# Kernel tuning notes

Measured on AMD Instinct MI355X. Metric: run time of the kernel, lower is better.

Reference implementation:

```python
import jax, jax.numpy as jnp
import numpy as np

B, T, H, K, C, U, IN = 128, 800, 512, 10, 80, 64, 3


def setup_inputs() -> dict:
    key = jax.random.key(0)
    ks = jax.random.split(key, 6)
    s = 0.08  # small init so exp() window params stay stable
    return {
        "strokes": jax.random.normal(ks[0], (B, T, IN), jnp.float32),
        "sentences": jax.random.randint(ks[1], (B, U), 0, C),
        "sentences_mask": jnp.ones((B, U), jnp.float32),
        "W_ih": jax.random.normal(ks[2], (4 * H, IN + C), jnp.float32) * s,
        "W_hh": jax.random.normal(ks[3], (4 * H, H), jnp.float32) * s,
        "b_ih": jnp.zeros((4 * H,), jnp.float32),
        "b_hh": jnp.zeros((4 * H,), jnp.float32),
        "W_win": jax.random.normal(ks[4], (3 * K, H), jnp.float32) * s,
        "b_win": jnp.zeros((3 * K,), jnp.float32),
    }


def reference(strokes, sentences, sentences_mask, W_ih, W_hh, b_ih, b_hh, W_win, b_win):
    # Pre-mask the one-hot character encoding: [B, U, C]
    onehot = jax.nn.one_hot(sentences, C, dtype=jnp.float32) * sentences_mask[:, :, None]
    u = jnp.arange(U, dtype=jnp.float32)  # character position grid
    bias = b_ih + b_hh

    def step(carry, x_t):
        h, c, kappa_prev, window = carry
        inp = jnp.concatenate([x_t, window], axis=-1)           # [B, IN+C]
        gates = inp @ W_ih.T + h @ W_hh.T + bias                 # [B, 4H]
        i, f, g, o = jnp.split(gates, 4, axis=-1)                # torch LSTMCell order i,f,g,o
        i, f, o = jax.nn.sigmoid(i), jax.nn.sigmoid(f), jax.nn.sigmoid(o)
        c = f * c + i * jnp.tanh(g)
        h = o * jnp.tanh(c)
        # Gaussian window parameters (eq. 48-51 in Graves 2013)
        p = h @ W_win.T + b_win                                  # [B, 3K]
        a_hat, b_hat, k_hat = jnp.split(p, 3, axis=-1)
        alpha = jnp.exp(a_hat)
        beta = jnp.exp(b_hat)
        kappa = kappa_prev + jnp.exp(k_hat)
        # phi[b,u] = sum_k alpha * exp(-beta * (kappa - u)^2)
        d = kappa[:, :, None] - u[None, None, :]                 # [B, K, U]
        phi = jnp.sum(alpha[:, :, None] * jnp.exp(-beta[:, :, None] * d * d), axis=1)  # [B, U]
        window = jnp.einsum('bu,buc->bc', phi, onehot)           # [B, C]
        return (h, c, kappa, window), (h, window, phi)

    init = (
        jnp.zeros((B, H), jnp.float32),
        jnp.zeros((B, H), jnp.float32),
        jnp.zeros((B, K), jnp.float32),
        jnp.zeros((B, C), jnp.float32),
    )
    xs = jnp.swapaxes(strokes, 0, 1)                             # [T, B, IN]
    _, (h_seq, w_seq, phi_seq) = jax.lax.scan(step, init, xs)
    return (
        jnp.swapaxes(h_seq, 0, 1),    # [B, T, H]
        jnp.swapaxes(w_seq, 0, 1),    # [B, T, C]
        jnp.swapaxes(phi_seq, 0, 1),  # [B, T, U]
    )
```

## Files before the change

### kernel.cpp

```cpp
#include <hip/hip_runtime.h>
#include <hip/hip_bf16.h>
#include <math.h>

#define B_   128
#define T_   800
#define H_   512
#define K_   10
#define C_   80
#define U_   64
#define IN_  3

#define NG   4
#define BPG  64
#define BT   32
#define NT   256
#define KROW 608
#define HB   512

#define WS_PACC_F  (2*B_*HB)
#define WS_BAR_F   (WS_PACC_F + NG*BT*30*2)
#define WS_TOTAL_F (WS_BAR_F + NG*8*32)

#define OFF_H    0ull
#define OFF_W    ((size_t)B_ * T_ * H_)
#define OFF_PHI  (OFF_W + (size_t)B_ * T_ * C_)

typedef __attribute__((ext_vector_type(8))) short short8;
typedef __attribute__((ext_vector_type(4))) float f32x4;

#define SWZB(row)    (((row) ^ ((row) >> 2)) & 3)
#define SWIDX(row,k) ((row)*KROW + ((((k) >> 3) ^ SWZB(row)) << 3) + ((k) & 7))
#define LDFRAG(arr,row,u) (*(const short8*)&(arr)[(row)*KROW + (((u) ^ SWZB(row)) << 3)])

__device__ __forceinline__ void stb_u32(unsigned* p, unsigned v) {
  asm volatile("global_store_dword %0, %1, off sc0 sc1" :: "v"(p), "v"(v) : "memory");
}
__device__ __forceinline__ void fence_vm() {
  asm volatile("s_waitcnt vmcnt(0)" ::: "memory");
}
__device__ __forceinline__ void flag_add(unsigned* p) {
  __hip_atomic_fetch_add(p, 1u, __ATOMIC_RELAXED, __HIP_MEMORY_SCOPE_AGENT);
}
__device__ __forceinline__ unsigned flag_ld(unsigned* p) {
  return __hip_atomic_load(p, __ATOMIC_RELAXED, __HIP_MEMORY_SCOPE_AGENT);
}
__device__ __forceinline__ void acq_fence(unsigned* p) {
  (void)__hip_atomic_load(p, __ATOMIC_ACQUIRE, __HIP_MEMORY_SCOPE_AGENT);
}
__device__ __forceinline__ float sigmoidf_(float v) { return 1.0f / (1.0f + expf(-v)); }
__device__ __forceinline__ unsigned pack_hl(float v) {
  unsigned hb = __float_as_uint(v) >> 16;
  float rs = v - __uint_as_float(hb << 16);
  unsigned lb = __float_as_uint(rs) >> 16;
  return (hb << 16) | lb;
}
__device__ __forceinline__ float comb_hl(short h, short l) {
  return __uint_as_float((unsigned)(unsigned short)h << 16) +
         __uint_as_float((unsigned)(unsigned short)l << 16);
}

__global__ void __launch_bounds__(256, 2)
init_ws_kernel(float* __restrict__ ws) {
  size_t i = (size_t)blockIdx.x * 256 + threadIdx.x;
  const size_t n = (size_t)WS_TOTAL_F;
  const size_t stride = (size_t)gridDim.x * 256;
  for (; i < n; i += stride) ws[i] = 0.0f;
}

__global__ void __launch_bounds__(NT, 1)
graves_kernel(const float* __restrict__ x,
              const int*   __restrict__ sent,
              const float* __restrict__ smask,
              const float* __restrict__ W_ih,
              const float* __restrict__ W_hh,
              const float* __restrict__ b_ih,
              const float* __restrict__ b_hh,
              const float* __restrict__ W_win,
              const float* __restrict__ b_win,
              float* __restrict__ out,
              float* __restrict__ ws)
{
  const int tid = threadIdx.x;
  const int bid = blockIdx.x;
  const int g   = bid >> 6;
  const int ub  = bid & (BPG - 1);
  const int b0  = g * BT;
  const int u0  = ub * 8;

  unsigned*  gbuf   = (unsigned*)ws;
  long long* pacc_g = (long long*)(ws + WS_PACC_F) + (size_t)g * (BT * 30);
  unsigned*  fb     = (unsigned*)(ws + WS_BAR_F) + (size_t)g * 256;
  unsigned*  c1l    = fb;

  __shared__ __align__(16) short whi[32 * KROW];
  __shared__ __align__(16) short wlo[32 * KROW];
  __shared__ __align__(16) short shi[32 * KROW];
  __shared__ __align__(16) short slo[32 * KROW];
  __shared__ float pbufS[32][32];
  __shared__ float hT[8 * 32];
  __shared__ float wwin[8 * 30];
  __shared__ float xwb[32 * 4];
  float* pbf = &pbufS[0][0];

  for (int idx = tid; idx < 32 * KROW; idx += NT) {
    const int r = idx / KROW, k = idx - r * KROW;
    const int uu = r >> 2, gate = r & 3, gr = gate * H_ + u0 + uu;
    float wv = 0.0f;
    if (k < H_)           wv = W_hh[(size_t)gr * H_ + k];
    else if (k < H_ + C_) wv = W_ih[(size_t)gr * (IN_ + C_) + IN_ + (k - H_)];
    const unsigned hb = __float_as_uint(wv) >> 16;
    const float rs = wv - __uint_as_float(hb << 16);
    const unsigned lb = __float_as_uint(rs) >> 16;
    const int li = SWIDX(r, k);
    whi[li] = (short)hb;
    wlo[li] = (short)lb;
  }
  for (int idx = tid; idx < 32 * 16; idx += NT) {
    const int b2 = idx >> 4, k = (H_ + C_) + (idx & 15);
    shi[SWIDX(b2, k)] = 0; slo[SWIDX(b2, k)] = 0;
  }
  if (tid < 32) {
    const int uu = tid >> 2, gate = tid & 3, gr = gate * H_ + u0 + uu;
    xwb[tid * 4 + 0] = W_ih[(size_t)gr * (IN_ + C_) + 0];
    xwb[tid * 4 + 1] = W_ih[(size_t)gr * (IN_ + C_) + 1];
    xwb[tid * 4 + 2] = W_ih[(size_t)gr * (IN_ + C_) + 2];
    xwb[tid * 4 + 3] = b_ih[gr] + b_hh[gr];
  }
  for (int idx = tid; idx < 240; idx += NT) {
    const int uu = idx / 30, j = idx - uu * 30;
    wwin[idx] = W_win[(size_t)j * H_ + u0 + uu];
  }

  const int lane = tid & 63;
  const int wid  = tid >> 6;
  const int ni   = wid & 1;
  const int kh   = wid >> 1;
  const int r16  = lane & 15;
  const int g4   = lane >> 4;
  const int bb   = ni * 16 + r16;

  const int pb = tid >> 3, ug = tid & 7;
  float msk[8]; int snt[8];
  #pragma unroll
  for (int i = 0; i < 8; ++i) {
    msk[i] = smask[(size_t)(b0 + pb) * U_ + ug * 8 + i];
    snt[i] = sent [(size_t)(b0 + pb) * U_ + ug * 8 + i];
  }
  const bool isWriter = (ub < BT);
  const int  wb_b = b0 + ub;
  __syncthreads();

  float cr0 = 0.0f, cr1 = 0.0f;
  long long prevp[4] = {0, 0, 0, 0};
  float kprevf[4] = {0.f, 0.f, 0.f, 0.f};

#define GSTEP(ks) { \
    const int uu_ = (ks) * 4 + g4; \
    const short8 bh = LDFRAG(shi, bb, uu_); \
    const short8 bl = LDFRAG(slo, bb, uu_); \
    const short8 ah0 = LDFRAG(whi, r16, uu_); \
    const short8 al0 = LDFRAG(wlo, r16, uu_); \
    const short8 ah1 = LDFRAG(whi, 16 + r16, uu_); \
    const short8 al1 = LDFRAG(wlo, 16 + r16, uu_); \
    a0 = __builtin_amdgcn_mfma_f32_16x16x32_bf16(ah0, bh, a0, 0, 0, 0); \
    a0 = __builtin_amdgcn_mfma_f32_16x16x32_bf16(ah0, bl, a0, 0, 0, 0); \
    a0 = __builtin_amdgcn_mfma_f32_16x16x32_bf16(al0, bh, a0, 0, 0, 0); \
    a1 = __builtin_amdgcn_mfma_f32_16x16x32_bf16(ah1, bh, a1, 0, 0, 0); \
    a1 = __builtin_amdgcn_mfma_f32_16x16x32_bf16(ah1, bl, a1, 0, 0, 0); \
    a1 = __builtin_amdgcn_mfma_f32_16x16x32_bf16(al1, bh, a1, 0, 0, 0); \
  }

  for (int t = 0; t <= T_; ++t) {
    if (t == T_ && !isWriter) break;

    const unsigned* pIn  = gbuf + (size_t)((t & 1) ^ 1) * (B_ * HB);
    unsigned*       pOut = gbuf + (size_t)(t & 1) * (B_ * HB);

    if (t > 0 && tid < 4) {
      unsigned* line = c1l + tid * 32;
      const unsigned tgt = 16u * (unsigned)t;
      while (flag_ld(line) < tgt) __builtin_amdgcn_s_sleep(1);
      acq_fence(line);
    }
    __syncthreads();

    float xv0 = 0.f, xv1 = 0.f, xv2 = 0.f;
    {
      const int sb = tid & 31, seg = tid >> 5;
      const unsigned* grow = pIn + (size_t)(b0 + sb) * HB + seg * 64;
      uint4 v[16];
      #pragma unroll
      for (int i = 0; i < 16; ++i) v[i] = *(const uint4*)(grow + i * 4);
      #pragma unroll
      for (int i = 0; i < 16; ++i) {
        const int k = seg * 64 + i * 4;
        const int idx = SWIDX(sb, k);
        const unsigned h01 = (v[i].x >> 16) | ((v[i].y >> 16) << 16);
        const unsigned h23 = (v[i].z >> 16) | ((v[i].w >> 16) << 16);
        const unsigned l01 = (v[i].x & 0xffffu) | ((v[i].y & 0xffffu) << 16);
        const unsigned l23 = (v[i].z & 0xffffu) | ((v[i].w & 0xffffu) << 16);
        *(uint2*)&shi[idx] = make_uint2(h01, h23);
        *(uint2*)&slo[idx] = make_uint2(l01, l23);
      }
      #pragma unroll
      for (int i = 0; i < 10; ++i) {
        const int c = seg * 10 + i;
        const int idx = SWIDX(sb, H_ + c);
        shi[idx] = 0; slo[idx] = 0;
      }
      if (kh == 0 && t < T_) {
        const float* xp = x + ((size_t)(b0 + bb) * T_ + t) * IN_;
        xv0 = xp[0]; xv1 = xp[1]; xv2 = xp[2];
      }
    }
    __syncthreads();

    if (t >= 1) {
      #pragma unroll
      for (int r = 0; r < 4; ++r) {
        const int item = tid + 256 * r;
        if (item < 960) {
          const int b = item / 30, j = item - b * 30;
          const long long v = pacc_g[b * 30 + j];
          const int hi = (int)(v >> 32);
          const unsigned lo = (unsigned)(v & 0xffffffffLL);
          const float pv = (float)hi + (float)lo * 0x1p-32f + b_win[j];
          float ev = __expf(pv);
          if (j >= 20) { ev += kprevf[r]; kprevf[r] = ev; }
          pbufS[b][j] = ev;
        }
      }
      __syncthreads();

      float al[10], be[10], ka[10];
      #pragma unroll
      for (int k2 = 0; k2 < 10; ++k2) {
        al[k2] = pbufS[pb][k2];
        be[k2] = pbufS[pb][10 + k2];
        ka[k2] = pbufS[pb][20 + k2];
      }
      float ph[8];
      #pragma unroll
      for (int i = 0; i < 8; ++i) {
        const float fu = (float)(ug * 8 + i);
        float s = 0.0f;
        #pragma unroll
        for (int k2 = 0; k2 < 10; ++k2) {
          const float d = ka[k2] - fu;
          s = fmaf(al[k2], __expf(-be[k2] * d * d), s);
        }
        ph[i] = s;
      }
      if (isWriter && pb == ub) {
        #pragma unroll
        for (int i = 0; i < 8; ++i)
          out[OFF_PHI + ((size_t)wb_b * T_ + (t - 1)) * U_ + ug * 8 + i] = ph[i];
      }
      #pragma unroll
      for (int i = 0; i < 8; ++i) ph[i] *= msk[i];

      #pragma unroll
      for (int r = 0; r < 8; ++r) {
        if (ug == r) {
          #pragma unroll
          for (int i = 0; i < 8; ++i) {
            const int idx = SWIDX(pb, H_ + snt[i]);
            float cur = comb_hl(shi[idx], slo[idx]) + ph[i];
            const unsigned pk = pack_hl(cur);
            shi[idx] = (short)(pk >> 16);
            slo[idx] = (short)(pk & 0xffffu);
          }
        }
        asm volatile("" ::: "memory");
      }
      __syncthreads();
      if (isWriter && tid < C_) {
        const int idx = SWIDX(ub, H_ + tid);
        out[OFF_W + ((size_t)wb_b * T_ + (t - 1)) * C_ + tid] = comb_hl(shi[idx], slo[idx]);
      }
    }
    if (t == T_) break;

    f32x4 a0 = {0.f, 0.f, 0.f, 0.f}, a1 = {0.f, 0.f, 0.f, 0.f};
    if (kh == 0) {
      #pragma unroll
      for (int ks = 0; ks < 8; ++ks) GSTEP(ks);
      GSTEP(16);
    } else {
      #pragma unroll
      for (int ks = 8; ks < 16; ++ks) GSTEP(ks);
      GSTEP(17); GSTEP(18);
    }

    __syncthreads();
    if (kh == 1) {
      #pragma unroll
      for (int e = 0; e < 4; ++e) {
        pbf[(ni * 2 + 0) * 256 + (g4 * 4 + e) * 16 + r16] = a0[e];
        pbf[(ni * 2 + 1) * 256 + (g4 * 4 + e) * 16 + r16] = a1[e];
      }
    }
    __syncthreads();
    if (kh == 0) {
      #pragma unroll
      for (int mi = 0; mi < 2; ++mi) {
        float ge[4];
        #pragma unroll
        for (int e = 0; e < 4; ++e) {
          const int r = mi * 16 + g4 * 4 + e;
          const float av = ((mi == 0) ? a0[e] : a1[e]) + pbf[(ni * 2 + mi) * 256 + (g4 * 4 + e) * 16 + r16];
          ge[e] = av + xwb[r*4+0]*xv0 + xwb[r*4+1]*xv1 + xwb[r*4+2]*xv2 + xwb[r*4+3];
        }
        const float iv = sigmoidf_(ge[0]);
        const float fv = sigmoidf_(ge[1]);
        const float gv = tanhf(ge[2]);
        const float ov = sigmoidf_(ge[3]);
        const float cprev = (mi == 0) ? cr0 : cr1;
        const float cv = fmaf(fv, cprev, iv * gv);
        if (mi == 0) cr0 = cv; else cr1 = cv;
        const float hv = ov * tanhf(cv);
        const int uu = mi * 4 + g4;
        hT[uu * 32 + bb] = hv;
        stb_u32(&pOut[(size_t)(b0 + bb) * HB + (u0 + uu)], pack_hl(hv));
        out[OFF_H + ((size_t)(b0 + bb) * T_ + t) * H_ + (u0 + uu)] = hv;
      }
    }
    __syncthreads();

    #pragma unroll
    for (int r = 0; r < 4; ++r) {
      const int item = tid + 256 * r;
      if (item < 960) {
        const int b = item / 30, j = item - b * 30;
        float s = 0.0f;
        #pragma unroll
        for (int uu = 0; uu < 8; ++uu) s = fmaf(wwin[uu * 30 + j], hT[uu * 32 + b], s);
        const long long nv = llrintf(s * 4294967296.0f);
        const unsigned long long d = (unsigned long long)(nv - prevp[r]);
        prevp[r] = nv;
        __hip_atomic_fetch_add((unsigned long long*)(pacc_g + b * 30 + j), d,
                               __ATOMIC_RELAXED, __HIP_MEMORY_SCOPE_AGENT);
      }
    }
    fence_vm();
    __syncthreads();
    if (tid == 0) flag_add(c1l + (ub & 3) * 32);
  }
#undef GSTEP
}

extern "C" void kernel_launch(void* const* d_in, const int* in_sizes, int n_in,
                              void* d_out, int out_size, void* d_ws, size_t ws_size,
                              hipStream_t stream) {
  const float* x     = (const float*)d_in[0];
  const int*   sent  = (const int*)  d_in[1];
  const float* smask = (const float*)d_in[2];
  const float* W_ih  = (const float*)d_in[3];
  const float* W_hh  = (const float*)d_in[4];
  const float* b_ih  = (const float*)d_in[5];
  const float* b_hh  = (const float*)d_in[6];
  const float* W_win = (const float*)d_in[7];
  const float* b_win = (const float*)d_in[8];
  float* ws  = (float*)d_ws;
  float* out = (float*)d_out;

  hipLaunchKernelGGL(init_ws_kernel, dim3(512), dim3(256), 0, stream, ws);
  hipLaunchKernelGGL(graves_kernel, dim3(NG * BPG), dim3(NT), 0, stream,
                     x, sent, smask, W_ih, W_hh, b_ih, b_hh, W_win, b_win, out, ws);
}
```

Before: 11.77 ms.

## Register-resident weights, sharded double-buffered window accumulators, wider flag lines

```diff
diff --git a/kernel.cpp b/kernel.cpp
--- a/kernel.cpp
+++ b/kernel.cpp
@@ -16,9 +16,10 @@
 #define NT   256
 #define KROW 608
 #define HB   512
+#define SHARDS 8
 
 #define WS_PACC_F  (2*B_*HB)
-#define WS_BAR_F   (WS_PACC_F + NG*BT*30*2)
+#define WS_BAR_F   (WS_PACC_F + 2*NG*SHARDS*960*2)
 #define WS_TOTAL_F (WS_BAR_F + NG*8*32)
 
 #define OFF_H    0ull
@@ -87,13 +88,11 @@
   const int b0  = g * BT;
   const int u0  = ub * 8;
 
-  unsigned*  gbuf   = (unsigned*)ws;
-  long long* pacc_g = (long long*)(ws + WS_PACC_F) + (size_t)g * (BT * 30);
-  unsigned*  fb     = (unsigned*)(ws + WS_BAR_F) + (size_t)g * 256;
-  unsigned*  c1l    = fb;
-
-  __shared__ __align__(16) short whi[32 * KROW];
-  __shared__ __align__(16) short wlo[32 * KROW];
+  unsigned*  gbuf      = (unsigned*)ws;
+  long long* pacc_base = (long long*)(ws + WS_PACC_F);
+  unsigned*  fb        = (unsigned*)(ws + WS_BAR_F) + (size_t)g * 256;
+  unsigned*  c1l       = fb;
+
   __shared__ __align__(16) short shi[32 * KROW];
   __shared__ __align__(16) short slo[32 * KROW];
   __shared__ float pbufS[32][32];
@@ -102,35 +101,6 @@
   __shared__ float xwb[32 * 4];
   float* pbf = &pbufS[0][0];
 
-  for (int idx = tid; idx < 32 * KROW; idx += NT) {
-    const int r = idx / KROW, k = idx - r * KROW;
-    const int uu = r >> 2, gate = r & 3, gr = gate * H_ + u0 + uu;
-    float wv = 0.0f;
-    if (k < H_)           wv = W_hh[(size_t)gr * H_ + k];
-    else if (k < H_ + C_) wv = W_ih[(size_t)gr * (IN_ + C_) + IN_ + (k - H_)];
-    const unsigned hb = __float_as_uint(wv) >> 16;
-    const float rs = wv - __uint_as_float(hb << 16);
-    const unsigned lb = __float_as_uint(rs) >> 16;
-    const int li = SWIDX(r, k);
-    whi[li] = (short)hb;
-    wlo[li] = (short)lb;
-  }
-  for (int idx = tid; idx < 32 * 16; idx += NT) {
-    const int b2 = idx >> 4, k = (H_ + C_) + (idx & 15);
-    shi[SWIDX(b2, k)] = 0; slo[SWIDX(b2, k)] = 0;
-  }
-  if (tid < 32) {
-    const int uu = tid >> 2, gate = tid & 3, gr = gate * H_ + u0 + uu;
-    xwb[tid * 4 + 0] = W_ih[(size_t)gr * (IN_ + C_) + 0];
-    xwb[tid * 4 + 1] = W_ih[(size_t)gr * (IN_ + C_) + 1];
-    xwb[tid * 4 + 2] = W_ih[(size_t)gr * (IN_ + C_) + 2];
-    xwb[tid * 4 + 3] = b_ih[gr] + b_hh[gr];
-  }
-  for (int idx = tid; idx < 240; idx += NT) {
-    const int uu = idx / 30, j = idx - uu * 30;
-    wwin[idx] = W_win[(size_t)j * H_ + u0 + uu];
-  }
-
   const int lane = tid & 63;
   const int wid  = tid >> 6;
   const int ni   = wid & 1;
@@ -139,6 +109,57 @@
   const int g4   = lane >> 4;
   const int bb   = ni * 16 + r16;
 
+  for (int idx = tid; idx < 32 * 16; idx += NT) {
+    const int b2 = idx >> 4, k = (H_ + C_) + (idx & 15);
+    shi[SWIDX(b2, k)] = 0; slo[SWIDX(b2, k)] = 0;
+  }
+  if (tid < 32) {
+    const int uu = tid >> 2, gate = tid & 3, gr = gate * H_ + u0 + uu;
+    xwb[tid * 4 + 0] = W_ih[(size_t)gr * (IN_ + C_) + 0];
+    xwb[tid * 4 + 1] = W_ih[(size_t)gr * (IN_ + C_) + 1];
+    xwb[tid * 4 + 2] = W_ih[(size_t)gr * (IN_ + C_) + 2];
+    xwb[tid * 4 + 3] = b_ih[gr] + b_hh[gr];
+  }
+  for (int idx = tid; idx < 240; idx += NT) {
+    const int uu = idx / 30, j = idx - uu * 30;
+    wwin[idx] = W_win[(size_t)j * H_ + u0 + uu];
+  }
+
+  short8 wah[10], wal[10], wbh[10], wbl[10];
+  {
+    const int uuA = r16 >> 2, gateA = r16 & 3;
+    const int grA = gateA * H_ + u0 + uuA;
+    const int grB = gateA * H_ + u0 + 4 + uuA;
+    #pragma unroll
+    for (int slot = 0; slot < 10; ++slot) {
+      int ks = 0; bool act;
+      if (kh == 0) { act = (slot < 9); ks = (slot < 8) ? slot : 16; }
+      else         { act = true;       ks = (slot < 8) ? (8 + slot) : ((slot == 8) ? 17 : 18); }
+      short8 h0 = {0,0,0,0,0,0,0,0}, l0 = h0, h1 = h0, l1 = h0;
+      if (act) {
+        #pragma unroll
+        for (int e = 0; e < 8; ++e) {
+          const int k = ks * 32 + g4 * 8 + e;
+          float wA = 0.f, wB = 0.f;
+          if (k < H_) {
+            wA = W_hh[(size_t)grA * H_ + k];
+            wB = W_hh[(size_t)grB * H_ + k];
+          } else if (k < H_ + C_) {
+            wA = W_ih[(size_t)grA * (IN_ + C_) + IN_ + (k - H_)];
+            wB = W_ih[(size_t)grB * (IN_ + C_) + IN_ + (k - H_)];
+          }
+          const unsigned ha = __float_as_uint(wA) >> 16;
+          const float ra = wA - __uint_as_float(ha << 16);
+          h0[e] = (short)ha; l0[e] = (short)(__float_as_uint(ra) >> 16);
+          const unsigned hbb = __float_as_uint(wB) >> 16;
+          const float rb = wB - __uint_as_float(hbb << 16);
+          h1[e] = (short)hbb; l1[e] = (short)(__float_as_uint(rb) >> 16);
+        }
+      }
+      wah[slot] = h0; wal[slot] = l0; wbh[slot] = h1; wbl[slot] = l1;
+    }
+  }
+
   const int pb = tid >> 3, ug = tid & 7;
   float msk[8]; int snt[8];
   #pragma unroll
@@ -151,24 +172,34 @@
   __syncthreads();
 
   float cr0 = 0.0f, cr1 = 0.0f;
-  long long prevp[4] = {0, 0, 0, 0};
   float kprevf[4] = {0.f, 0.f, 0.f, 0.f};
-
-#define GSTEP(ks) { \
-    const int uu_ = (ks) * 4 + g4; \
+  long long pA0 = 0, pA1 = 0, pA2 = 0, pA3 = 0;
+  long long pB0 = 0, pB1 = 0, pB2 = 0, pB3 = 0;
+
+#define GSTEP(slot, ksv) { \
+    const int uu_ = (ksv) * 4 + g4; \
     const short8 bh = LDFRAG(shi, bb, uu_); \
     const short8 bl = LDFRAG(slo, bb, uu_); \
-    const short8 ah0 = LDFRAG(whi, r16, uu_); \
-    const short8 al0 = LDFRAG(wlo, r16, uu_); \
-    const short8 ah1 = LDFRAG(whi, 16 + r16, uu_); \
-    const short8 al1 = LDFRAG(wlo, 16 + r16, uu_); \
-    a0 = __builtin_amdgcn_mfma_f32_16x16x32_bf16(ah0, bh, a0, 0, 0, 0); \
-    a0 = __builtin_amdgcn_mfma_f32_16x16x32_bf16(ah0, bl, a0, 0, 0, 0); \
-    a0 = __builtin_amdgcn_mfma_f32_16x16x32_bf16(al0, bh, a0, 0, 0, 0); \
-    a1 = __builtin_amdgcn_mfma_f32_16x16x32_bf16(ah1, bh, a1, 0, 0, 0); \
-    a1 = __builtin_amdgcn_mfma_f32_16x16x32_bf16(ah1, bl, a1, 0, 0, 0); \
-    a1 = __builtin_amdgcn_mfma_f32_16x16x32_bf16(al1, bh, a1, 0, 0, 0); \
-  }
+    a0 = __builtin_amdgcn_mfma_f32_16x16x32_bf16(wah[slot], bh, a0, 0, 0, 0); \
+    a0 = __builtin_amdgcn_mfma_f32_16x16x32_bf16(wah[slot], bl, a0, 0, 0, 0); \
+    a0 = __builtin_amdgcn_mfma_f32_16x16x32_bf16(wal[slot], bh, a0, 0, 0, 0); \
+    a1 = __builtin_amdgcn_mfma_f32_16x16x32_bf16(wbh[slot], bh, a1, 0, 0, 0); \
+    a1 = __builtin_amdgcn_mfma_f32_16x16x32_bf16(wbh[slot], bl, a1, 0, 0, 0); \
+    a1 = __builtin_amdgcn_mfma_f32_16x16x32_bf16(wbl[slot], bh, a1, 0, 0, 0); \
+  }
+
+#define PUB1(r, PREV) { \
+    const int item = tid + 256 * (r); \
+    if (item < 960) { \
+      const int b2 = item / 30, j = item - b2 * 30; \
+      float s = 0.f; \
+      _Pragma("unroll") \
+      for (int uu = 0; uu < 8; ++uu) s = fmaf(wwin[uu * 30 + j], hT[uu * 32 + b2], s); \
+      const long long nv = llrintf(s * 4294967296.0f); \
+      const unsigned long long d = (unsigned long long)(nv - (PREV)); \
+      (PREV) = nv; \
+      __hip_atomic_fetch_add(paccW + item, d, __ATOMIC_RELAXED, __HIP_MEMORY_SCOPE_AGENT); \
+    } }
 
   for (int t = 0; t <= T_; ++t) {
     if (t == T_ && !isWriter) break;
@@ -176,9 +207,9 @@
     const unsigned* pIn  = gbuf + (size_t)((t & 1) ^ 1) * (B_ * HB);
     unsigned*       pOut = gbuf + (size_t)(t & 1) * (B_ * HB);
 
-    if (t > 0 && tid < 4) {
+    if (t > 0 && tid < 8) {
       unsigned* line = c1l + tid * 32;
-      const unsigned tgt = 16u * (unsigned)t;
+      const unsigned tgt = 8u * (unsigned)t;
       while (flag_ld(line) < tgt) __builtin_amdgcn_s_sleep(1);
       acq_fence(line);
     }
@@ -216,18 +247,21 @@
     __syncthreads();
 
     if (t >= 1) {
+      const long long* paccR = pacc_base + ((size_t)(((t - 1) & 1) * NG + g) * SHARDS) * 960;
       #pragma unroll
       for (int r = 0; r < 4; ++r) {
         const int item = tid + 256 * r;
         if (item < 960) {
-          const int b = item / 30, j = item - b * 30;
-          const long long v = pacc_g[b * 30 + j];
+          long long v = 0;
+          #pragma unroll
+          for (int sh = 0; sh < SHARDS; ++sh) v += paccR[(size_t)sh * 960 + item];
           const int hi = (int)(v >> 32);
           const unsigned lo = (unsigned)(v & 0xffffffffLL);
+          const int b2 = item / 30, j = item - b2 * 30;
           const float pv = (float)hi + (float)lo * 0x1p-32f + b_win[j];
           float ev = __expf(pv);
           if (j >= 20) { ev += kprevf[r]; kprevf[r] = ev; }
-          pbufS[b][j] = ev;
+          pbufS[b2][j] = ev;
         }
       }
       __syncthreads();
@@ -283,13 +317,13 @@
 
     f32x4 a0 = {0.f, 0.f, 0.f, 0.f}, a1 = {0.f, 0.f, 0.f, 0.f};
     if (kh == 0) {
-      #pragma unroll
-      for (int ks = 0; ks < 8; ++ks) GSTEP(ks);
-      GSTEP(16);
+      GSTEP(0, 0) GSTEP(1, 1) GSTEP(2, 2) GSTEP(3, 3)
+      GSTEP(4, 4) GSTEP(5, 5) GSTEP(6, 6) GSTEP(7, 7)
+      GSTEP(8, 16)
     } else {
-      #pragma unroll
-      for (int ks = 8; ks < 16; ++ks) GSTEP(ks);
-      GSTEP(17); GSTEP(18);
+      GSTEP(0, 8)  GSTEP(1, 9)  GSTEP(2, 10) GSTEP(3, 11)
+      GSTEP(4, 12) GSTEP(5, 13) GSTEP(6, 14) GSTEP(7, 15)
+      GSTEP(8, 17) GSTEP(9, 18)
     }
 
     __syncthreads();
@@ -322,31 +356,30 @@
         const int uu = mi * 4 + g4;
         hT[uu * 32 + bb] = hv;
         stb_u32(&pOut[(size_t)(b0 + bb) * HB + (u0 + uu)], pack_hl(hv));
-        out[OFF_H + ((size_t)(b0 + bb) * T_ + t) * H_ + (u0 + uu)] = hv;
-      }
-    }
-    __syncthreads();
-
-    #pragma unroll
-    for (int r = 0; r < 4; ++r) {
-      const int item = tid + 256 * r;
-      if (item < 960) {
-        const int b = item / 30, j = item - b * 30;
-        float s = 0.0f;
-        #pragma unroll
-        for (int uu = 0; uu < 8; ++uu) s = fmaf(wwin[uu * 30 + j], hT[uu * 32 + b], s);
-        const long long nv = llrintf(s * 4294967296.0f);
-        const unsigned long long d = (unsigned long long)(nv - prevp[r]);
-        prevp[r] = nv;
-        __hip_atomic_fetch_add((unsigned long long*)(pacc_g + b * 30 + j), d,
-                               __ATOMIC_RELAXED, __HIP_MEMORY_SCOPE_AGENT);
-      }
+      }
+    }
+    __syncthreads();
+
+    {
+      unsigned long long* paccW = (unsigned long long*)
+          (pacc_base + ((size_t)((t & 1) * NG + g) * SHARDS + (ub & 7)) * 960);
+      if (t & 1) { PUB1(0, pB0) PUB1(1, pB1) PUB1(2, pB2) PUB1(3, pB3) }
+      else       { PUB1(0, pA0) PUB1(1, pA1) PUB1(2, pA2) PUB1(3, pA3) }
     }
     fence_vm();
     __syncthreads();
-    if (tid == 0) flag_add(c1l + (ub & 3) * 32);
+    if (tid == 0) flag_add(c1l + (ub & 7) * 32);
+
+    if (kh == 0) {
+      #pragma unroll
+      for (int mi = 0; mi < 2; ++mi) {
+        const int uu = mi * 4 + g4;
+        out[OFF_H + ((size_t)(b0 + bb) * T_ + t) * H_ + (u0 + uu)] = hT[uu * 32 + bb];
+      }
+    }
   }
 #undef GSTEP
+#undef PUB1
 }
 
 extern "C" void kernel_launch(void* const* d_in, const int* in_sizes, int n_in,
```

Measured after the change: 16.36 ms. +39.1%, slower.

## Repartition recurrence into fewer larger blocks with register-resident weights

Applied to the files above, without the earlier changes.

```diff
diff --git a/kernel.cpp b/kernel.cpp
--- a/kernel.cpp
+++ b/kernel.cpp
@@ -11,15 +11,15 @@
 #define IN_  3
 
 #define NG   4
-#define BPG  64
+#define BPG  16
 #define BT   32
-#define NT   256
+#define NT   512
 #define KROW 608
 #define HB   512
 
-#define WS_PACC_F  (2*B_*HB)
-#define WS_BAR_F   (WS_PACC_F + NG*BT*30*2)
-#define WS_TOTAL_F (WS_BAR_F + NG*8*32)
+#define WS_PPS_F   (2*B_*HB)
+#define WS_BAR_F   (WS_PPS_F + 2*NG*BPG*960)
+#define WS_TOTAL_F (WS_BAR_F + NG*4*32)
 
 #define OFF_H    0ull
 #define OFF_W    ((size_t)B_ * T_ * H_)
@@ -35,14 +35,21 @@
 __device__ __forceinline__ void stb_u32(unsigned* p, unsigned v) {
   asm volatile("global_store_dword %0, %1, off sc0 sc1" :: "v"(p), "v"(v) : "memory");
 }
+__device__ __forceinline__ void stb_f32(float* p, float v) {
+  asm volatile("global_store_dword %0, %1, off sc0 sc1" :: "v"(p), "v"(v) : "memory");
+}
 __device__ __forceinline__ void fence_vm() {
   asm volatile("s_waitcnt vmcnt(0)" ::: "memory");
 }
 __device__ __forceinline__ void flag_add(unsigned* p) {
   __hip_atomic_fetch_add(p, 1u, __ATOMIC_RELAXED, __HIP_MEMORY_SCOPE_AGENT);
 }
-__device__ __forceinline__ unsigned flag_ld(unsigned* p) {
-  return __hip_atomic_load(p, __ATOMIC_RELAXED, __HIP_MEMORY_SCOPE_AGENT);
+__device__ __forceinline__ unsigned flag_sum4(unsigned* base) {
+  unsigned s0 = __hip_atomic_load(base +  0, __ATOMIC_RELAXED, __HIP_MEMORY_SCOPE_AGENT);
+  unsigned s1 = __hip_atomic_load(base + 32, __ATOMIC_RELAXED, __HIP_MEMORY_SCOPE_AGENT);
+  unsigned s2 = __hip_atomic_load(base + 64, __ATOMIC_RELAXED, __HIP_MEMORY_SCOPE_AGENT);
+  unsigned s3 = __hip_atomic_load(base + 96, __ATOMIC_RELAXED, __HIP_MEMORY_SCOPE_AGENT);
+  return (s0 + s1) + (s2 + s3);
 }
 __device__ __forceinline__ void acq_fence(unsigned* p) {
   (void)__hip_atomic_load(p, __ATOMIC_ACQUIRE, __HIP_MEMORY_SCOPE_AGENT);
@@ -67,7 +74,7 @@
   for (; i < n; i += stride) ws[i] = 0.0f;
 }
 
-__global__ void __launch_bounds__(NT, 1)
+__global__ void __launch_bounds__(NT, 2)
 graves_kernel(const float* __restrict__ x,
               const int*   __restrict__ sent,
               const float* __restrict__ smask,
@@ -82,153 +89,157 @@
 {
   const int tid = threadIdx.x;
   const int bid = blockIdx.x;
-  const int g   = bid >> 6;
-  const int ub  = bid & (BPG - 1);
-  const int b0  = g * BT;
-  const int u0  = ub * 8;
-
-  unsigned*  gbuf   = (unsigned*)ws;
-  long long* pacc_g = (long long*)(ws + WS_PACC_F) + (size_t)g * (BT * 30);
-  unsigned*  fb     = (unsigned*)(ws + WS_BAR_F) + (size_t)g * 256;
-  unsigned*  c1l    = fb;
-
-  __shared__ __align__(16) short whi[32 * KROW];
-  __shared__ __align__(16) short wlo[32 * KROW];
+  const int xcd  = bid & 7, slot = bid >> 3;
+  const int g    = xcd >> 1;
+  const int ub   = ((xcd & 1) << 3) | slot;
+  const int b0   = g * BT;
+  const int u0   = ub * 32;
+
+  unsigned* gbuf = (unsigned*)ws;
+  float*    pps  = ws + WS_PPS_F;
+  unsigned* c1l  = (unsigned*)(ws + WS_BAR_F) + (size_t)g * 128;
+
   __shared__ __align__(16) short shi[32 * KROW];
   __shared__ __align__(16) short slo[32 * KROW];
   __shared__ float pbufS[32][32];
-  __shared__ float hT[8 * 32];
-  __shared__ float wwin[8 * 30];
-  __shared__ float xwb[32 * 4];
-  float* pbf = &pbufS[0][0];
-
-  for (int idx = tid; idx < 32 * KROW; idx += NT) {
-    const int r = idx / KROW, k = idx - r * KROW;
-    const int uu = r >> 2, gate = r & 3, gr = gate * H_ + u0 + uu;
-    float wv = 0.0f;
-    if (k < H_)           wv = W_hh[(size_t)gr * H_ + k];
-    else if (k < H_ + C_) wv = W_ih[(size_t)gr * (IN_ + C_) + IN_ + (k - H_)];
-    const unsigned hb = __float_as_uint(wv) >> 16;
-    const float rs = wv - __uint_as_float(hb << 16);
-    const unsigned lb = __float_as_uint(rs) >> 16;
-    const int li = SWIDX(r, k);
-    whi[li] = (short)hb;
-    wlo[li] = (short)lb;
-  }
+  __shared__ float hT[32 * 32];
+  __shared__ float wwin[32 * 30];
+  __shared__ float xwb[128][4];
+
+  const int lane = tid & 63;
+  const int wid  = tid >> 6;
+  const int r16  = lane & 15;
+  const int g4   = lane >> 4;
+
   for (int idx = tid; idx < 32 * 16; idx += NT) {
     const int b2 = idx >> 4, k = (H_ + C_) + (idx & 15);
     shi[SWIDX(b2, k)] = 0; slo[SWIDX(b2, k)] = 0;
   }
-  if (tid < 32) {
+  if (tid < 128) {
     const int uu = tid >> 2, gate = tid & 3, gr = gate * H_ + u0 + uu;
-    xwb[tid * 4 + 0] = W_ih[(size_t)gr * (IN_ + C_) + 0];
-    xwb[tid * 4 + 1] = W_ih[(size_t)gr * (IN_ + C_) + 1];
-    xwb[tid * 4 + 2] = W_ih[(size_t)gr * (IN_ + C_) + 2];
-    xwb[tid * 4 + 3] = b_ih[gr] + b_hh[gr];
-  }
-  for (int idx = tid; idx < 240; idx += NT) {
+    xwb[tid][0] = W_ih[(size_t)gr * (IN_ + C_) + 0];
+    xwb[tid][1] = W_ih[(size_t)gr * (IN_ + C_) + 1];
+    xwb[tid][2] = W_ih[(size_t)gr * (IN_ + C_) + 2];
+    xwb[tid][3] = b_ih[gr] + b_hh[gr];
+  }
+  for (int idx = tid; idx < 32 * 30; idx += NT) {
     const int uu = idx / 30, j = idx - uu * 30;
     wwin[idx] = W_win[(size_t)j * H_ + u0 + uu];
   }
 
-  const int lane = tid & 63;
-  const int wid  = tid >> 6;
-  const int ni   = wid & 1;
-  const int kh   = wid >> 1;
-  const int r16  = lane & 15;
-  const int g4   = lane >> 4;
-  const int bb   = ni * 16 + r16;
-
-  const int pb = tid >> 3, ug = tid & 7;
-  float msk[8]; int snt[8];
+  short8 wh[19], wl[19];
+  {
+    const int lrow = wid * 16 + r16;
+    const int uuA = lrow >> 2, gateA = lrow & 3;
+    const int gr = gateA * H_ + u0 + uuA;
+    #pragma unroll
+    for (int ks = 0; ks < 19; ++ks) {
+      short8 h8 = {0,0,0,0,0,0,0,0}, l8 = h8;
+      #pragma unroll
+      for (int e = 0; e < 8; ++e) {
+        const int k = ks * 32 + g4 * 8 + e;
+        float wv = 0.0f;
+        if (k < H_)           wv = W_hh[(size_t)gr * H_ + k];
+        else if (k < H_ + C_) wv = W_ih[(size_t)gr * (IN_ + C_) + IN_ + (k - H_)];
+        const unsigned hb = __float_as_uint(wv) >> 16;
+        const float rs = wv - __uint_as_float(hb << 16);
+        h8[e] = (short)hb; l8[e] = (short)(__float_as_uint(rs) >> 16);
+      }
+      wh[ks] = h8; wl[ks] = l8;
+    }
+  }
+
+  const int pb = tid >> 4, q = tid & 15;
+  float msk[4]; int snt[4];
   #pragma unroll
-  for (int i = 0; i < 8; ++i) {
-    msk[i] = smask[(size_t)(b0 + pb) * U_ + ug * 8 + i];
-    snt[i] = sent [(size_t)(b0 + pb) * U_ + ug * 8 + i];
-  }
-  const bool isWriter = (ub < BT);
-  const int  wb_b = b0 + ub;
+  for (int i = 0; i < 4; ++i) {
+    msk[i] = smask[(size_t)(b0 + pb) * U_ + q * 4 + i];
+    snt[i] = sent [(size_t)(b0 + pb) * U_ + q * 4 + i];
+  }
   __syncthreads();
 
   float cr0 = 0.0f, cr1 = 0.0f;
-  long long prevp[4] = {0, 0, 0, 0};
-  float kprevf[4] = {0.f, 0.f, 0.f, 0.f};
+  float kp0 = 0.0f, kp1 = 0.0f;
 
 #define GSTEP(ks) { \
     const int uu_ = (ks) * 4 + g4; \
-    const short8 bh = LDFRAG(shi, bb, uu_); \
-    const short8 bl = LDFRAG(slo, bb, uu_); \
-    const short8 ah0 = LDFRAG(whi, r16, uu_); \
-    const short8 al0 = LDFRAG(wlo, r16, uu_); \
-    const short8 ah1 = LDFRAG(whi, 16 + r16, uu_); \
-    const short8 al1 = LDFRAG(wlo, 16 + r16, uu_); \
-    a0 = __builtin_amdgcn_mfma_f32_16x16x32_bf16(ah0, bh, a0, 0, 0, 0); \
-    a0 = __builtin_amdgcn_mfma_f32_16x16x32_bf16(ah0, bl, a0, 0, 0, 0); \
-    a0 = __builtin_amdgcn_mfma_f32_16x16x32_bf16(al0, bh, a0, 0, 0, 0); \
-    a1 = __builtin_amdgcn_mfma_f32_16x16x32_bf16(ah1, bh, a1, 0, 0, 0); \
-    a1 = __builtin_amdgcn_mfma_f32_16x16x32_bf16(ah1, bl, a1, 0, 0, 0); \
-    a1 = __builtin_amdgcn_mfma_f32_16x16x32_bf16(al1, bh, a1, 0, 0, 0); \
+    const short8 bh0 = LDFRAG(shi, r16, uu_); \
+    const short8 bl0 = LDFRAG(slo, r16, uu_); \
+    const short8 bh1 = LDFRAG(shi, 16 + r16, uu_); \
+    const short8 bl1 = LDFRAG(slo, 16 + r16, uu_); \
+    a0 = __builtin_amdgcn_mfma_f32_16x16x32_bf16(wh[ks], bh0, a0, 0, 0, 0); \
+    a0 = __builtin_amdgcn_mfma_f32_16x16x32_bf16(wh[ks], bl0, a0, 0, 0, 0); \
+    a0 = __builtin_amdgcn_mfma_f32_16x16x32_bf16(wl[ks], bh0, a0, 0, 0, 0); \
+    a1 = __builtin_amdgcn_mfma_f32_16x16x32_bf16(wh[ks], bh1, a1, 0, 0, 0); \
+    a1 = __builtin_amdgcn_mfma_f32_16x16x32_bf16(wh[ks], bl1, a1, 0, 0, 0); \
+    a1 = __builtin_amdgcn_mfma_f32_16x16x32_bf16(wl[ks], bh1, a1, 0, 0, 0); \
   }
 
   for (int t = 0; t <= T_; ++t) {
-    if (t == T_ && !isWriter) break;
-
     const unsigned* pIn  = gbuf + (size_t)((t & 1) ^ 1) * (B_ * HB);
     unsigned*       pOut = gbuf + (size_t)(t & 1) * (B_ * HB);
 
-    if (t > 0 && tid < 4) {
-      unsigned* line = c1l + tid * 32;
+    if (t > 0 && tid == 0) {
       const unsigned tgt = 16u * (unsigned)t;
-      while (flag_ld(line) < tgt) __builtin_amdgcn_s_sleep(1);
-      acq_fence(line);
+      while (flag_sum4(c1l) < tgt) __builtin_amdgcn_s_sleep(1);
+      acq_fence(c1l);
     }
     __syncthreads();
 
-    float xv0 = 0.f, xv1 = 0.f, xv2 = 0.f;
+    float xv00=0.f,xv01=0.f,xv02=0.f, xv10=0.f,xv11=0.f,xv12=0.f;
     {
       const int sb = tid & 31, seg = tid >> 5;
-      const unsigned* grow = pIn + (size_t)(b0 + sb) * HB + seg * 64;
-      uint4 v[16];
-      #pragma unroll
-      for (int i = 0; i < 16; ++i) v[i] = *(const uint4*)(grow + i * 4);
-      #pragma unroll
-      for (int i = 0; i < 16; ++i) {
-        const int k = seg * 64 + i * 4;
-        const int idx = SWIDX(sb, k);
-        const unsigned h01 = (v[i].x >> 16) | ((v[i].y >> 16) << 16);
-        const unsigned h23 = (v[i].z >> 16) | ((v[i].w >> 16) << 16);
-        const unsigned l01 = (v[i].x & 0xffffu) | ((v[i].y & 0xffffu) << 16);
-        const unsigned l23 = (v[i].z & 0xffffu) | ((v[i].w & 0xffffu) << 16);
-        *(uint2*)&shi[idx] = make_uint2(h01, h23);
-        *(uint2*)&slo[idx] = make_uint2(l01, l23);
-      }
-      #pragma unroll
-      for (int i = 0; i < 10; ++i) {
-        const int c = seg * 10 + i;
+      if (t < T_) {
+        const uint4* grow = (const uint4*)(pIn + (size_t)(b0 + sb) * HB + seg * 32);
+        uint4 v[8];
+        #pragma unroll
+        for (int i = 0; i < 8; ++i) v[i] = grow[i];
+        #pragma unroll
+        for (int i = 0; i < 8; ++i) {
+          const int k = seg * 32 + i * 4;
+          const int idx = SWIDX(sb, k);
+          const unsigned h01 = (v[i].x >> 16) | ((v[i].y >> 16) << 16);
+          const unsigned h23 = (v[i].z >> 16) | ((v[i].w >> 16) << 16);
+          const unsigned l01 = (v[i].x & 0xffffu) | ((v[i].y & 0xffffu) << 16);
+          const unsigned l23 = (v[i].z & 0xffffu) | ((v[i].w & 0xffffu) << 16);
+          *(uint2*)&shi[idx] = make_uint2(h01, h23);
+          *(uint2*)&slo[idx] = make_uint2(l01, l23);
+        }
+        const float* xp0 = x + ((size_t)(b0 + r16) * T_ + t) * IN_;
+        const float* xp1 = x + ((size_t)(b0 + 16 + r16) * T_ + t) * IN_;
+        xv00 = xp0[0]; xv01 = xp0[1]; xv02 = xp0[2];
+        xv10 = xp1[0]; xv11 = xp1[1]; xv12 = xp1[2];
+      }
+      #pragma unroll
+      for (int i = 0; i < 5; ++i) {
+        const int c = seg * 5 + i;
         const int idx = SWIDX(sb, H_ + c);
         shi[idx] = 0; slo[idx] = 0;
       }
-      if (kh == 0 && t < T_) {
-        const float* xp = x + ((size_t)(b0 + bb) * T_ + t) * IN_;
-        xv0 = xp[0]; xv1 = xp[1]; xv2 = xp[2];
-      }
     }
     __syncthreads();
 
     if (t >= 1) {
-      #pragma unroll
-      for (int r = 0; r < 4; ++r) {
-        const int item = tid + 256 * r;
-        if (item < 960) {
-          const int b = item / 30, j = item - b * 30;
-          const long long v = pacc_g[b * 30 + j];
-          const int hi = (int)(v >> 32);
-          const unsigned lo = (unsigned)(v & 0xffffffffLL);
-          const float pv = (float)hi + (float)lo * 0x1p-32f + b_win[j];
-          float ev = __expf(pv);
-          if (j >= 20) { ev += kprevf[r]; kprevf[r] = ev; }
-          pbufS[b][j] = ev;
-        }
+      const float* ppsR = pps + (size_t)(((t - 1) & 1) * NG + g) * (BPG * 960);
+      {
+        const int item = tid;
+        const int b2 = item / 30, j = item - b2 * 30;
+        float v = 0.0f;
+        #pragma unroll
+        for (int sh = 0; sh < BPG; ++sh) v += ppsR[sh * 960 + item];
+        float ev = __expf(v + b_win[j]);
+        if (j >= 20) { ev += kp0; kp0 = ev; }
+        pbufS[b2][j] = ev;
+      }
+      if (tid < 448) {
+        const int item = tid + 512;
+        const int b2 = item / 30, j = item - b2 * 30;
+        float v = 0.0f;
+        #pragma unroll
+        for (int sh = 0; sh < BPG; ++sh) v += ppsR[sh * 960 + item];
+        float ev = __expf(v + b_win[j]);
+        if (j >= 20) { ev += kp1; kp1 = ev; }
+        pbufS[b2][j] = ev;
       }
       __syncthreads();
 
@@ -239,10 +250,10 @@
         be[k2] = pbufS[pb][10 + k2];
         ka[k2] = pbufS[pb][20 + k2];
       }
-      float ph[8];
-      #pragma unroll
-      for (int i = 0; i < 8; ++i) {
-        const float fu = (float)(ug * 8 + i);
+      float ph[4];
+      #pragma unroll
+      for (int i = 0; i < 4; ++i) {
+        const float fu = (float)(q * 4 + i);
         float s = 0.0f;
         #pragma unroll
         for (int k2 = 0; k2 < 10; ++k2) {
@@ -251,19 +262,19 @@
         }
         ph[i] = s;
       }
-      if (isWriter && pb == ub) {
-        #pragma unroll
-        for (int i = 0; i < 8; ++i)
-          out[OFF_PHI + ((size_t)wb_b * T_ + (t - 1)) * U_ + ug * 8 + i] = ph[i];
-      }
-      #pragma unroll
-      for (int i = 0; i < 8; ++i) ph[i] *= msk[i];
-
-      #pragma unroll
-      for (int r = 0; r < 8; ++r) {
-        if (ug == r) {
+      if ((pb >> 1) == ub) {
+        #pragma unroll
+        for (int i = 0; i < 4; ++i)
+          out[OFF_PHI + ((size_t)(b0 + pb) * T_ + (t - 1)) * U_ + q * 4 + i] = ph[i];
+      }
+      #pragma unroll
+      for (int i = 0; i < 4; ++i) ph[i] *= msk[i];
+
+      #pragma unroll
+      for (int r = 0; r < 16; ++r) {
+        if (q == r) {
           #pragma unroll
-          for (int i = 0; i < 8; ++i) {
+          for (int i = 0; i < 4; ++i) {
             const int idx = SWIDX(pb, H_ + snt[i]);
             float cur = comb_hl(shi[idx], slo[idx]) + ph[i];
             const unsigned pk = pack_hl(cur);
@@ -274,77 +285,74 @@
         asm volatile("" ::: "memory");
       }
       __syncthreads();
-      if (isWriter && tid < C_) {
-        const int idx = SWIDX(ub, H_ + tid);
-        out[OFF_W + ((size_t)wb_b * T_ + (t - 1)) * C_ + tid] = comb_hl(shi[idx], slo[idx]);
+      if (tid < 2 * C_) {
+        const int lb = 2 * ub + tid / C_, c = tid % C_;
+        const int idx = SWIDX(lb, H_ + c);
+        out[OFF_W + ((size_t)(b0 + lb) * T_ + (t - 1)) * C_ + c] = comb_hl(shi[idx], slo[idx]);
       }
     }
     if (t == T_) break;
 
     f32x4 a0 = {0.f, 0.f, 0.f, 0.f}, a1 = {0.f, 0.f, 0.f, 0.f};
-    if (kh == 0) {
-      #pragma unroll
-      for (int ks = 0; ks < 8; ++ks) GSTEP(ks);
-      GSTEP(16);
-    } else {
-      #pragma unroll
-      for (int ks = 8; ks < 16; ++ks) GSTEP(ks);
-      GSTEP(17); GSTEP(18);
-    }
-
-    __syncthreads();
-    if (kh == 1) {
-      #pragma unroll
-      for (int e = 0; e < 4; ++e) {
-        pbf[(ni * 2 + 0) * 256 + (g4 * 4 + e) * 16 + r16] = a0[e];
-        pbf[(ni * 2 + 1) * 256 + (g4 * 4 + e) * 16 + r16] = a1[e];
-      }
-    }
-    __syncthreads();
-    if (kh == 0) {
-      #pragma unroll
-      for (int mi = 0; mi < 2; ++mi) {
+    GSTEP(0)  GSTEP(1)  GSTEP(2)  GSTEP(3)  GSTEP(4)
+    GSTEP(5)  GSTEP(6)  GSTEP(7)  GSTEP(8)  GSTEP(9)
+    GSTEP(10) GSTEP(11) GSTEP(12) GSTEP(13) GSTEP(14)
+    GSTEP(15) GSTEP(16) GSTEP(17) GSTEP(18)
+
+    {
+      const int unit = wid * 4 + g4;
+      const int prow = wid * 16 + g4 * 4;
+      #pragma unroll
+      for (int bt2 = 0; bt2 < 2; ++bt2) {
+        const f32x4 acc = bt2 ? a1 : a0;
+        const int batch = bt2 * 16 + r16;
+        const float X0 = bt2 ? xv10 : xv00, X1 = bt2 ? xv11 : xv01, X2 = bt2 ? xv12 : xv02;
         float ge[4];
         #pragma unroll
-        for (int e = 0; e < 4; ++e) {
-          const int r = mi * 16 + g4 * 4 + e;
-          const float av = ((mi == 0) ? a0[e] : a1[e]) + pbf[(ni * 2 + mi) * 256 + (g4 * 4 + e) * 16 + r16];
-          ge[e] = av + xwb[r*4+0]*xv0 + xwb[r*4+1]*xv1 + xwb[r*4+2]*xv2 + xwb[r*4+3];
-        }
+        for (int e = 0; e < 4; ++e)
+          ge[e] = acc[e] + xwb[prow+e][0]*X0 + xwb[prow+e][1]*X1 + xwb[prow+e][2]*X2 + xwb[prow+e][3];
         const float iv = sigmoidf_(ge[0]);
         const float fv = sigmoidf_(ge[1]);
         const float gv = tanhf(ge[2]);
         const float ov = sigmoidf_(ge[3]);
-        const float cprev = (mi == 0) ? cr0 : cr1;
+        const float cprev = bt2 ? cr1 : cr0;
         const float cv = fmaf(fv, cprev, iv * gv);
-        if (mi == 0) cr0 = cv; else cr1 = cv;
+        if (bt2) cr1 = cv; else cr0 = cv;
         const float hv = ov * tanhf(cv);
-        const int uu = mi * 4 + g4;
-        hT[uu * 32 + bb] = hv;
-        stb_u32(&pOut[(size_t)(b0 + bb) * HB + (u0 + uu)], pack_hl(hv));
-        out[OFF_H + ((size_t)(b0 + bb) * T_ + t) * H_ + (u0 + uu)] = hv;
+        hT[unit * 32 + batch] = hv;
+        stb_u32(&pOut[(size_t)(b0 + batch) * HB + u0 + unit], pack_hl(hv));
       }
     }
     __syncthreads();
 
-    #pragma unroll
-    for (int r = 0; r < 4; ++r) {
-      const int item = tid + 256 * r;
-      if (item < 960) {
-        const int b = item / 30, j = item - b * 30;
+    {
+      float* ppsW = pps + (size_t)((t & 1) * NG + g) * (BPG * 960) + (size_t)ub * 960;
+      {
+        const int item = tid;
+        const int b2 = item / 30, j = item - b2 * 30;
         float s = 0.0f;
         #pragma unroll
-        for (int uu = 0; uu < 8; ++uu) s = fmaf(wwin[uu * 30 + j], hT[uu * 32 + b], s);
-        const long long nv = llrintf(s * 4294967296.0f);
-        const unsigned long long d = (unsigned long long)(nv - prevp[r]);
-        prevp[r] = nv;
-        __hip_atomic_fetch_add((unsigned long long*)(pacc_g + b * 30 + j), d,
-                               __ATOMIC_RELAXED, __HIP_MEMORY_SCOPE_AGENT);
+        for (int uu = 0; uu < 32; ++uu) s = fmaf(wwin[uu * 30 + j], hT[uu * 32 + b2], s);
+        stb_f32(ppsW + item, s);
+      }
+      if (tid < 448) {
+        const int item = tid + 512;
+        const int b2 = item / 30, j = item - b2 * 30;
+        float s = 0.0f;
+        #pragma unroll
+        for (int uu = 0; uu < 32; ++uu) s = fmaf(wwin[uu * 30 + j], hT[uu * 32 + b2], s);
+        stb_f32(ppsW + item, s);
       }
     }
     fence_vm();
     __syncthreads();
     if (tid == 0) flag_add(c1l + (ub & 3) * 32);
+
+    {
+      const int b3 = tid >> 4, u2 = (tid & 15) * 2;
+      float2 hv2 = make_float2(hT[u2 * 32 + b3], hT[(u2 + 1) * 32 + b3]);
+      *(float2*)&out[OFF_H + ((size_t)(b0 + b3) * T_ + t) * H_ + u0 + u2] = hv2;
+    }
   }
 #undef GSTEP
 }
```

Result: slower. 19.13 ms (+62.6%).
